# Performance work log

Measured on AMD Instinct MI355X. Metric: run time of the kernel, lower is better.

Reference implementation:

```python
import jax, jax.numpy as jnp
import numpy as np

B, C, H, W = 8, 256, 64, 64
CI = 128  # inter_channels
EPS = 1e-5

def conv1x1(x, w, b):
    # x:[B,C,H,W], w:[O,C], b:[O] -> [B,O,H,W]
    return jnp.einsum('bchw,oc->bohw', x, w) + b[None, :, None, None]

def maxpool2(t):
    b, c, h, w = t.shape
    return t.reshape(b, c, h // 2, 2, w // 2, 2).max(axis=(3, 5))

def setup_inputs() -> dict:
    key = jax.random.key(0)
    ks = jax.random.split(key, 11)
    s_in = 1.0 / np.sqrt(C)
    s_ci = 1.0 / np.sqrt(CI)
    return {
        'x':        jax.random.normal(ks[0], (B, C, H, W), jnp.float32),
        'g_w':      jax.random.normal(ks[1], (CI, C), jnp.float32) * s_in,
        'g_b':      jax.random.normal(ks[2], (CI,), jnp.float32) * s_in,
        'theta_w':  jax.random.normal(ks[3], (CI, C), jnp.float32) * s_in,
        'theta_b':  jax.random.normal(ks[4], (CI,), jnp.float32) * s_in,
        'phi_w':    jax.random.normal(ks[5], (CI, C), jnp.float32) * s_in,
        'phi_b':    jax.random.normal(ks[6], (CI,), jnp.float32) * s_in,
        'w_w':      jax.random.normal(ks[7], (C, CI), jnp.float32) * s_ci,
        'w_b':      jax.random.normal(ks[8], (C,), jnp.float32) * s_ci,
        'bn_gamma': jax.random.normal(ks[9], (C,), jnp.float32) * 0.1 + 1.0,
        'bn_beta':  jax.random.normal(ks[10], (C,), jnp.float32) * 0.1,
    }

def reference(x, g_w, g_b, theta_w, theta_b, phi_w, phi_b, w_w, w_b, bn_gamma, bn_beta):
    b, c, h, w = x.shape
    n = h * w
    # g and phi are sub-sampled with 2x2 max pool -> Ns = n // 4
    g_x = maxpool2(conv1x1(x, g_w, g_b)).reshape(b, CI, -1)      # [B,CI,Ns]
    g_x = g_x.transpose(0, 2, 1)                                  # [B,Ns,CI]
    theta_x = conv1x1(x, theta_w, theta_b).reshape(b, CI, n)
    theta_x = theta_x.transpose(0, 2, 1)                          # [B,N,CI]
    phi_x = maxpool2(conv1x1(x, phi_w, phi_b)).reshape(b, CI, -1)  # [B,CI,Ns]
    f = jnp.einsum('bnc,bcm->bnm', theta_x, phi_x)                # [B,N,Ns] (no 1/sqrt(d) scale, faithful)
    f_div_c = jax.nn.softmax(f, axis=-1)
    y = jnp.einsum('bnm,bmc->bnc', f_div_c, g_x)                  # [B,N,CI]
    y = y.transpose(0, 2, 1).reshape(b, CI, h, w)
    wy = conv1x1(y, w_w, w_b)                                     # [B,C,H,W]
    # BatchNorm2d in training mode: batch stats over (B,H,W)
    mean = wy.mean(axis=(0, 2, 3), keepdims=True)
    var = wy.var(axis=(0, 2, 3), keepdims=True)
    wy_bn = (wy - mean) * jax.lax.rsqrt(var + EPS)
    wy_bn = wy_bn * bn_gamma[None, :, None, None] + bn_beta[None, :, None, None]
    return wy_bn + x
```

## Files before the change

### kernel.cpp

```cpp
#include <hip/hip_runtime.h>
#include <hip/hip_bf16.h>
#include <hip/hip_fp16.h>
#include <math.h>

#define B 8
#define C 256
#define HH 64
#define WW 64
#define NN 4096
#define CI 128
#define NS 1024
#define EPS 1e-5f

typedef __attribute__((ext_vector_type(8))) _Float16 f16x8;
typedef __attribute__((ext_vector_type(4))) float f32x4;

static __device__ __forceinline__ unsigned short f2h_bits(float f) {
    return __half_as_ushort(__float2half(f));
}
static __device__ __forceinline__ float h2f(unsigned short u) {
    return __half2float(__ushort_as_half(u));
}

__global__ __launch_bounds__(256) void k_xt(const float* __restrict__ x,
        unsigned short* __restrict__ xh,
        const float* __restrict__ tw, const float* __restrict__ pw,
        const float* __restrict__ gw, const float* __restrict__ ww,
        unsigned short* __restrict__ wh) {
    int tid = threadIdx.x;
    if (blockIdx.x == 64) {
        int inst = blockIdx.y * B + blockIdx.z;
        int base = inst * 4096;
        #pragma unroll
        for (int k = 0; k < 16; ++k) {
            int idx = base + tid + k * 256;
            int sel = idx >> 15, off = idx & 32767;
            const float* src = (sel == 0) ? tw : (sel == 1) ? pw : (sel == 2) ? gw : ww;
            wh[idx] = f2h_bits(src[off]);
        }
        return;
    }
    __shared__ float s_t[64 * 65];
    int n0 = blockIdx.x * 64;
    int c0 = blockIdx.y * 64;
    int b  = blockIdx.z;
    #pragma unroll
    for (int k = 0; k < 16; ++k) {
        int idx = tid + k * 256;
        int cl = idx >> 6, nl = idx & 63;
        s_t[cl * 65 + nl] = x[((size_t)b * C + c0 + cl) * NN + n0 + nl];
    }
    __syncthreads();
    #pragma unroll
    for (int k = 0; k < 8; ++k) {
        int idx = tid + k * 256;
        int nl = idx >> 5, cp = (idx & 31) * 2;
        ushort2 o;
        o.x = f2h_bits(s_t[cp * 65 + nl]);
        o.y = f2h_bits(s_t[(cp + 1) * 65 + nl]);
        *(ushort2*)&xh[((size_t)b * NN + n0 + nl) * C + c0 + cp] = o;
    }
}

__global__ __launch_bounds__(512) void k_convs(const unsigned short* __restrict__ xh,
        const unsigned short* __restrict__ twh, const unsigned short* __restrict__ pwh,
        const unsigned short* __restrict__ gwh,
        const float* __restrict__ tb, const float* __restrict__ pb, const float* __restrict__ gb_,
        unsigned short* __restrict__ theta, unsigned short* __restrict__ phi,
        unsigned short* __restrict__ gout) {
    int blk = blockIdx.x;
    int b   = blk >> 5;
    int mh  = blk & 31;
    int tid = threadIdx.x;
    int lane = tid & 63, wv = tid >> 6;
    int lr = lane & 15, lh = lane >> 4;
    int wn = wv & 3, wc = wv >> 2;
    size_t row0 = (size_t)blk * 128;

    f32x4 accT[8];
    f32x4 aP0[4], aP1[4], aG0[4], aG1[4];
    #pragma unroll
    for (int i = 0; i < 8; ++i) accT[i] = (f32x4){0,0,0,0};
    #pragma unroll
    for (int i = 0; i < 4; ++i) {
        aP0[i] = (f32x4){0,0,0,0}; aP1[i] = (f32x4){0,0,0,0};
        aG0[i] = (f32x4){0,0,0,0}; aG1[i] = (f32x4){0,0,0,0};
    }

    const unsigned short* ap0 = xh + (row0 + wn * 16 + lr) * C + lh * 8;
    const unsigned short* ap1 = ap0 + (size_t)64 * C;
    #pragma unroll
    for (int kc = 0; kc < 8; ++kc) {
        f16x8 a0 = *(const f16x8*)(ap0 + kc * 32);
        f16x8 a1 = *(const f16x8*)(ap1 + kc * 32);
        f16x8 aT = (wv < 4) ? a0 : a1;
        #pragma unroll
        for (int ct = 0; ct < 8; ++ct) {
            f16x8 bt_ = *(const f16x8*)&twh[(ct * 16 + lr) * C + kc * 32 + lh * 8];
            accT[ct] = __builtin_amdgcn_mfma_f32_16x16x32_f16(aT, bt_, accT[ct], 0, 0, 0);
        }
        #pragma unroll
        for (int ct = 0; ct < 4; ++ct) {
            int wrow = (wc * 64 + ct * 16 + lr) * C + kc * 32 + lh * 8;
            f16x8 bp = *(const f16x8*)&pwh[wrow];
            f16x8 bg = *(const f16x8*)&gwh[wrow];
            aP0[ct] = __builtin_amdgcn_mfma_f32_16x16x32_f16(a0, bp, aP0[ct], 0, 0, 0);
            aP1[ct] = __builtin_amdgcn_mfma_f32_16x16x32_f16(a1, bp, aP1[ct], 0, 0, 0);
            aG0[ct] = __builtin_amdgcn_mfma_f32_16x16x32_f16(a0, bg, aG0[ct], 0, 0, 0);
            aG1[ct] = __builtin_amdgcn_mfma_f32_16x16x32_f16(a1, bg, aG1[ct], 0, 0, 0);
        }
    }
    #pragma unroll
    for (int ct = 0; ct < 8; ++ct) {
        int ci = ct * 16 + lr;
        float bias = tb[ci];
        #pragma unroll
        for (int r = 0; r < 4; ++r)
            theta[(row0 + wv * 16 + lh * 4 + r) * CI + ci] = f2h_bits(accT[ct][r] + bias);
    }
    #pragma unroll
    for (int ct = 0; ct < 4; ++ct) {
        int ci = wc * 64 + ct * 16 + lr;
        float biasP = pb[ci], biasG = gb_[ci];
        #pragma unroll
        for (int j = 0; j < 2; ++j) {
            int m = mh * 32 + wn * 8 + lh * 2 + j;
            float vP = fmaxf(fmaxf(aP0[ct][2*j], aP0[ct][2*j+1]),
                             fmaxf(aP1[ct][2*j], aP1[ct][2*j+1])) + biasP;
            float vG = fmaxf(fmaxf(aG0[ct][2*j], aG0[ct][2*j+1]),
                             fmaxf(aG1[ct][2*j], aG1[ct][2*j+1])) + biasG;
            phi[((size_t)b * NS + m) * CI + ci]  = f2h_bits(vP);
            gout[((size_t)b * CI + ci) * NS + m] = f2h_bits(vG);
        }
    }
}

#define SPH 136
#define SG  72
#define SP  72
__global__ __launch_bounds__(256, 3) void k_attn_mfma(const unsigned short* __restrict__ theta,
        const unsigned short* __restrict__ phi, const unsigned short* __restrict__ g,
        unsigned short* __restrict__ yp, float2* __restrict__ ml) {
    __shared__ unsigned short s_ph[64 * SPH];
    __shared__ unsigned short s_g[128 * SG];
    __shared__ unsigned short s_p[64 * SP];
    int rb = blockIdx.x;
    int b  = blockIdx.y;
    int sx = blockIdx.z;
    int tid = threadIdx.x;
    int lane = tid & 63, wv = tid >> 6;
    int lr = lane & 15, lh = lane >> 4;
    int row0 = rb * 64;
    int wrow = wv * 16;

    f16x8 a_th[4];
    {
        const unsigned short* tp = theta + ((size_t)b * NN + row0 + wrow + lr) * CI + lh * 8;
        #pragma unroll
        for (int kc = 0; kc < 4; ++kc) a_th[kc] = *(const f16x8*)(tp + kc * 32);
    }

    f32x4 yacc[8];
    #pragma unroll
    for (int i = 0; i < 8; ++i) yacc[i] = (f32x4){0.f, 0.f, 0.f, 0.f};
    float mrun[4] = {-1e30f, -1e30f, -1e30f, -1e30f};
    float lrun[4] = {0.f, 0.f, 0.f, 0.f};

    for (int t = 0; t < 8; ++t) {
        int mt = sx * 8 + t;
        __syncthreads();
        {
            const ushort4* src = (const ushort4*)(phi + ((size_t)b * NS + mt * 64) * CI);
            #pragma unroll
            for (int k = 0; k < 8; ++k) {
                int tt = tid + k * 256;
                int r = tt >> 5, cq = tt & 31;
                ushort4 vv = src[r * 32 + cq];
                *(ushort4*)&s_ph[r * SPH + cq * 4] = vv;
            }
            const ushort4* sg = (const ushort4*)(g + (size_t)b * CI * NS);
            #pragma unroll
            for (int k = 0; k < 8; ++k) {
                int tt = tid + k * 256;
                int ci = tt >> 4, cq = tt & 15;
                ushort4 vv = sg[ci * 256 + mt * 16 + cq];
                *(ushort4*)&s_g[ci * SG + cq * 4] = vv;
            }
        }
        __syncthreads();

        f32x4 S[4];
        #pragma unroll
        for (int nt = 0; nt < 4; ++nt) S[nt] = (f32x4){0.f, 0.f, 0.f, 0.f};
        #pragma unroll
        for (int nt = 0; nt < 4; ++nt) {
            #pragma unroll
            for (int kc = 0; kc < 4; ++kc) {
                f16x8 bf = *(const f16x8*)&s_ph[(nt * 16 + lr) * SPH + kc * 32 + lh * 8];
                S[nt] = __builtin_amdgcn_mfma_f32_16x16x32_f16(a_th[kc], bf, S[nt], 0, 0, 0);
            }
        }

        float rmax[4], rs[4], scale[4];
        #pragma unroll
        for (int r = 0; r < 4; ++r)
            rmax[r] = fmaxf(fmaxf(S[0][r], S[1][r]), fmaxf(S[2][r], S[3][r]));
        #pragma unroll
        for (int s = 1; s < 16; s <<= 1) {
            #pragma unroll
            for (int r = 0; r < 4; ++r) rmax[r] = fmaxf(rmax[r], __shfl_xor(rmax[r], s));
        }
        #pragma unroll
        for (int r = 0; r < 4; ++r) {
            float mnew = fmaxf(mrun[r], rmax[r]);
            scale[r] = __expf(mrun[r] - mnew);
            mrun[r] = mnew;
            rs[r] = 0.f;
        }
        #pragma unroll
        for (int nt = 0; nt < 4; ++nt) {
            #pragma unroll
            for (int r = 0; r < 4; ++r) {
                float e = __expf(S[nt][r] - mrun[r]);
                S[nt][r] = e;
                rs[r] += e;
            }
        }
        #pragma unroll
        for (int s = 1; s < 16; s <<= 1) {
            #pragma unroll
            for (int r = 0; r < 4; ++r) rs[r] += __shfl_xor(rs[r], s);
        }
        #pragma unroll
        for (int r = 0; r < 4; ++r) lrun[r] = lrun[r] * scale[r] + rs[r];
        #pragma unroll
        for (int i = 0; i < 8; ++i) {
            #pragma unroll
            for (int r = 0; r < 4; ++r) yacc[i][r] *= scale[r];
        }
        #pragma unroll
        for (int nt = 0; nt < 4; ++nt) {
            #pragma unroll
            for (int r = 0; r < 4; ++r)
                s_p[(wrow + lh * 4 + r) * SP + nt * 16 + lr] = f2h_bits(S[nt][r]);
        }

        f16x8 a_p[2];
        #pragma unroll
        for (int kc = 0; kc < 2; ++kc)
            a_p[kc] = *(const f16x8*)&s_p[(wrow + lr) * SP + kc * 32 + lh * 8];
        #pragma unroll
        for (int ct = 0; ct < 8; ++ct) {
            #pragma unroll
            for (int kc = 0; kc < 2; ++kc) {
                f16x8 bg = *(const f16x8*)&s_g[(ct * 16 + lr) * SG + kc * 32 + lh * 8];
                yacc[ct] = __builtin_amdgcn_mfma_f32_16x16x32_f16(a_p[kc], bg, yacc[ct], 0, 0, 0);
            }
        }
    }

    size_t pbase = ((size_t)(sx * B + b) * NN + row0 + wrow);
    #pragma unroll
    for (int ct = 0; ct < 8; ++ct) {
        #pragma unroll
        for (int r = 0; r < 4; ++r)
            yp[(pbase + lh * 4 + r) * CI + ct * 16 + lr] = f2h_bits(yacc[ct][r]);
    }
    if (lr == 0) {
        #pragma unroll
        for (int r = 0; r < 4; ++r) {
            float2 v; v.x = mrun[r]; v.y = lrun[r];
            ml[pbase + lh * 4 + r] = v;
        }
    }
}

__global__ __launch_bounds__(256) void k_wconv(const unsigned short* __restrict__ yp,
        const float2* __restrict__ ml, const unsigned short* __restrict__ wwh,
        const float* __restrict__ wb, unsigned short* __restrict__ wyh,
        float* __restrict__ psum, float* __restrict__ psq) {
    int blk = blockIdx.x;
    int b   = blk >> 6;
    int nloc = (blk & 63) * 64;
    int tid = threadIdx.x;
    int lane = tid & 63, wv = tid >> 6;
    int lr = lane & 15, lh = lane >> 4;

    f32x4 acc[4][4];
    #pragma unroll
    for (int i = 0; i < 4; ++i)
        #pragma unroll
        for (int j = 0; j < 4; ++j) acc[i][j] = (f32x4){0.f, 0.f, 0.f, 0.f};

    const unsigned short* y0b = yp + ((size_t)b * NN + nloc) * CI;
    const unsigned short* y1b = yp + ((size_t)(B + b) * NN + nloc) * CI;
    const float2* ml0 = ml + ((size_t)b * NN + nloc);
    const float2* ml1 = ml + ((size_t)(B + b) * NN + nloc);

    float a0v[4], a1v[4];
    #pragma unroll
    for (int bt = 0; bt < 4; ++bt) {
        int n = bt * 16 + lr;
        float2 p0 = ml0[n], p1 = ml1[n];
        float M = fmaxf(p0.x, p1.x);
        float e0 = __expf(p0.x - M), e1 = __expf(p1.x - M);
        float L = e0 * p0.y + e1 * p1.y;
        a0v[bt] = e0 / L;
        a1v[bt] = e1 / L;
    }

    #pragma unroll
    for (int kc = 0; kc < 4; ++kc) {
        f16x8 a[4], bf[4];
        #pragma unroll
        for (int at = 0; at < 4; ++at)
            a[at] = *(const f16x8*)&wwh[(wv * 64 + at * 16 + lr) * CI + kc * 32 + lh * 8];
        #pragma unroll
        for (int bt = 0; bt < 4; ++bt) {
            size_t off = (size_t)(bt * 16 + lr) * CI + kc * 32 + lh * 8;
            f16x8 u0 = *(const f16x8*)&y0b[off];
            f16x8 u1 = *(const f16x8*)&y1b[off];
            f16x8 v;
            #pragma unroll
            for (int i = 0; i < 8; ++i)
                v[i] = (_Float16)(a0v[bt] * (float)u0[i] + a1v[bt] * (float)u1[i]);
            bf[bt] = v;
        }
        #pragma unroll
        for (int at = 0; at < 4; ++at)
            #pragma unroll
            for (int bt = 0; bt < 4; ++bt)
                acc[at][bt] = __builtin_amdgcn_mfma_f32_16x16x32_f16(a[at], bf[bt], acc[at][bt], 0, 0, 0);
    }
    #pragma unroll
    for (int at = 0; at < 4; ++at) {
        #pragma unroll
        for (int r = 0; r < 4; ++r) {
            int co = wv * 64 + at * 16 + lh * 4 + r;
            float bias = wb[co];
            unsigned short* wp = wyh + ((size_t)b * C + co) * NN + nloc;
            float sv = 0.f, q = 0.f;
            #pragma unroll
            for (int bt = 0; bt < 4; ++bt) {
                float v = acc[at][bt][r] + bias;
                wp[bt * 16 + lr] = f2h_bits(v);
                sv += v;
                q = fmaf(v, v, q);
            }
            #pragma unroll
            for (int o = 1; o < 16; o <<= 1) {
                sv += __shfl_xor(sv, o);
                q  += __shfl_xor(q, o);
            }
            if (lr == 0) {
                psum[co * 512 + blk] = sv;
                psq[co * 512 + blk]  = q;
            }
        }
    }
}

__global__ __launch_bounds__(64) void k_stats_r(const float* __restrict__ psum,
        const float* __restrict__ psq, float* __restrict__ stats) {
    int c = blockIdx.x;
    int lane = threadIdx.x;
    float s = 0.f, q = 0.f;
    #pragma unroll
    for (int k = 0; k < 8; ++k) {
        s += psum[c * 512 + lane + k * 64];
        q += psq[c * 512 + lane + k * 64];
    }
    #pragma unroll
    for (int o = 32; o >= 1; o >>= 1) {
        s += __shfl_down(s, o);
        q += __shfl_down(q, o);
    }
    if (lane == 0) { stats[c] = s; stats[256 + c] = q; }
}

__global__ __launch_bounds__(256) void k_bn_out(const unsigned short* __restrict__ wyh,
        const float* __restrict__ x, const float* __restrict__ stats,
        const float* __restrict__ gamma, const float* __restrict__ beta,
        float* __restrict__ out) {
    size_t t = (size_t)blockIdx.x * 256 + threadIdx.x;
    size_t base = t * 8;
    int c = (int)((base >> 12) & 255);
    float mean = stats[c] * (1.f / 32768.f);
    float var  = stats[256 + c] * (1.f / 32768.f) - mean * mean;
    float sc = gamma[c] * rsqrtf(var + EPS);
    float sh = beta[c] - mean * sc;
    ushort4 w0 = *(const ushort4*)&wyh[base];
    ushort4 w1 = *(const ushort4*)&wyh[base + 4];
    float4 x0 = *(const float4*)&x[base];
    float4 x1 = *(const float4*)&x[base + 4];
    float4 o0, o1;
    o0.x = fmaf(h2f(w0.x), sc, sh) + x0.x;
    o0.y = fmaf(h2f(w0.y), sc, sh) + x0.y;
    o0.z = fmaf(h2f(w0.z), sc, sh) + x0.z;
    o0.w = fmaf(h2f(w0.w), sc, sh) + x0.w;
    o1.x = fmaf(h2f(w1.x), sc, sh) + x1.x;
    o1.y = fmaf(h2f(w1.y), sc, sh) + x1.y;
    o1.z = fmaf(h2f(w1.z), sc, sh) + x1.z;
    o1.w = fmaf(h2f(w1.w), sc, sh) + x1.w;
    *(float4*)&out[base]     = o0;
    *(float4*)&out[base + 4] = o1;
}

extern "C" void kernel_launch(void* const* d_in, const int* in_sizes, int n_in,
                              void* d_out, int out_size, void* d_ws, size_t ws_size,
                              hipStream_t stream) {
    const float* x    = (const float*)d_in[0];
    const float* g_w  = (const float*)d_in[1];
    const float* g_b  = (const float*)d_in[2];
    const float* th_w = (const float*)d_in[3];
    const float* th_b = (const float*)d_in[4];
    const float* ph_w = (const float*)d_in[5];
    const float* ph_b = (const float*)d_in[6];
    const float* w_w  = (const float*)d_in[7];
    const float* w_b  = (const float*)d_in[8];
    const float* bn_g = (const float*)d_in[9];
    const float* bn_b = (const float*)d_in[10];
    float* out = (float*)d_out;

    char* w0 = (char*)d_ws;
    unsigned short* xh    = (unsigned short*)w0;
    unsigned short* yp    = (unsigned short*)w0;
    unsigned short* theta = (unsigned short*)(w0 + 16777216);
    unsigned short* wh    = (unsigned short*)(w0 + 25165824);
    unsigned short* twh   = wh;
    unsigned short* pwh   = wh + 32768;
    unsigned short* gwh   = wh + 65536;
    unsigned short* wwh   = wh + 98304;
    unsigned short* phi   = (unsigned short*)(w0 + 25427968);
    unsigned short* gx    = (unsigned short*)(w0 + 27525120);
    unsigned short* wyh   = (unsigned short*)(w0 + 38010880);
    float*          psum  = (float*)(w0 + 54788096);
    float*          psq   = (float*)(w0 + 55312384);
    float*          stats = (float*)(w0 + 55836672);
    float2*         ml    = (float2*)(w0 + 55840768);

    k_xt<<<dim3(65, 4, B), 256, 0, stream>>>(x, xh, th_w, ph_w, g_w, w_w, wh);
    k_convs<<<256, 512, 0, stream>>>(xh, twh, pwh, gwh, th_b, ph_b, g_b, theta, phi, gx);
    k_attn_mfma<<<dim3(64, B, 2), 256, 0, stream>>>(theta, phi, gx, yp, ml);
    k_wconv<<<512, 256, 0, stream>>>(yp, ml, wwh, w_b, wyh, psum, psq);
    k_stats_r<<<256, 64, 0, stream>>>(psum, psq, stats);
    k_bn_out<<<4096, 256, 0, stream>>>(wyh, x, stats, bn_g, bn_b, out);
}
```

Measured before the change: 135.6 us.

## Prefetch next phi/g tile into registers during MFMA compute in attention kernel

Global loads of the phi and g tiles for the next iteration now go into registers before the current tile's MFMA work, and are written to shared memory after it. The goal is to hide global-memory latency behind compute instead of stalling at the top of each iteration. s_setprio also raises wave priority around the MFMA blocks. This costs 16 extra ushort4 registers per thread, which may lower occupancy.

```diff
diff --git a/kernel.cpp b/kernel.cpp
--- a/kernel.cpp
+++ b/kernel.cpp
@@ -160,38 +160,44 @@
         for (int kc = 0; kc < 4; ++kc) a_th[kc] = *(const f16x8*)(tp + kc * 32);
     }
 
+    const ushort4* phsrc = (const ushort4*)(phi + (size_t)b * NS * CI);
+    const ushort4* gsrc  = (const ushort4*)(g + (size_t)b * CI * NS);
+
+    ushort4 rph[8], rg[8];
+    auto issue = [&](int mt) {
+        #pragma unroll
+        for (int k = 0; k < 8; ++k) {
+            int tt = tid + k * 256;
+            rph[k] = phsrc[(mt * 64 + (tt >> 5)) * 32 + (tt & 31)];
+            rg[k]  = gsrc[(tt >> 4) * 256 + mt * 16 + (tt & 15)];
+        }
+    };
+    auto commit = [&]() {
+        #pragma unroll
+        for (int k = 0; k < 8; ++k) {
+            int tt = tid + k * 256;
+            *(ushort4*)&s_ph[(tt >> 5) * SPH + (tt & 31) * 4] = rph[k];
+            *(ushort4*)&s_g[(tt >> 4) * SG + (tt & 15) * 4]   = rg[k];
+        }
+    };
+
     f32x4 yacc[8];
     #pragma unroll
     for (int i = 0; i < 8; ++i) yacc[i] = (f32x4){0.f, 0.f, 0.f, 0.f};
     float mrun[4] = {-1e30f, -1e30f, -1e30f, -1e30f};
     float lrun[4] = {0.f, 0.f, 0.f, 0.f};
 
+    issue(sx * 8);
+    commit();
+    __syncthreads();
+
     for (int t = 0; t < 8; ++t) {
-        int mt = sx * 8 + t;
-        __syncthreads();
-        {
-            const ushort4* src = (const ushort4*)(phi + ((size_t)b * NS + mt * 64) * CI);
-            #pragma unroll
-            for (int k = 0; k < 8; ++k) {
-                int tt = tid + k * 256;
-                int r = tt >> 5, cq = tt & 31;
-                ushort4 vv = src[r * 32 + cq];
-                *(ushort4*)&s_ph[r * SPH + cq * 4] = vv;
-            }
-            const ushort4* sg = (const ushort4*)(g + (size_t)b * CI * NS);
-            #pragma unroll
-            for (int k = 0; k < 8; ++k) {
-                int tt = tid + k * 256;
-                int ci = tt >> 4, cq = tt & 15;
-                ushort4 vv = sg[ci * 256 + mt * 16 + cq];
-                *(ushort4*)&s_g[ci * SG + cq * 4] = vv;
-            }
-        }
-        __syncthreads();
+        if (t < 7) issue(sx * 8 + t + 1);
 
         f32x4 S[4];
         #pragma unroll
         for (int nt = 0; nt < 4; ++nt) S[nt] = (f32x4){0.f, 0.f, 0.f, 0.f};
+        __builtin_amdgcn_s_setprio(1);
         #pragma unroll
         for (int nt = 0; nt < 4; ++nt) {
             #pragma unroll
@@ -200,6 +206,7 @@
                 S[nt] = __builtin_amdgcn_mfma_f32_16x16x32_f16(a_th[kc], bf, S[nt], 0, 0, 0);
             }
         }
+        __builtin_amdgcn_s_setprio(0);
 
         float rmax[4], rs[4], scale[4];
         #pragma unroll
@@ -249,6 +256,7 @@
         #pragma unroll
         for (int kc = 0; kc < 2; ++kc)
             a_p[kc] = *(const f16x8*)&s_p[(wrow + lr) * SP + kc * 32 + lh * 8];
+        __builtin_amdgcn_s_setprio(1);
         #pragma unroll
         for (int ct = 0; ct < 8; ++ct) {
             #pragma unroll
@@ -256,6 +264,13 @@
                 f16x8 bg = *(const f16x8*)&s_g[(ct * 16 + lr) * SG + kc * 32 + lh * 8];
                 yacc[ct] = __builtin_amdgcn_mfma_f32_16x16x32_f16(a_p[kc], bg, yacc[ct], 0, 0, 0);
             }
+        }
+        __builtin_amdgcn_s_setprio(0);
+
+        __syncthreads();
+        if (t < 7) {
+            commit();
+            __syncthreads();
         }
     }
 
```

Measured after the change: 136.5 us. No clear change (+0.6%).

## Split attention key dimension four ways and merge partials in output conv

Applied to the files above, without the earlier changes.

The flash-attention kernel now splits the key/value dimension into four chunks instead of two, doubling the grid to 2048 blocks with half as many tiles per block. The output 1x1 conv kernel merges four partial results using the stored max and sum values. The workspace layout is reshuffled so the larger partial-output buffer fits. The intent is more parallelism and occupancy in attention. The cost is twice the partial-output write and read traffic and more merge work in the conv kernel.

```diff
diff --git a/kernel.cpp b/kernel.cpp
--- a/kernel.cpp
+++ b/kernel.cpp
@@ -11,6 +11,7 @@
 #define CI 128
 #define NS 1024
 #define EPS 1e-5f
+#define MSPLIT 4
 
 typedef __attribute__((ext_vector_type(8))) _Float16 f16x8;
 typedef __attribute__((ext_vector_type(4))) float f32x4;
@@ -166,8 +167,8 @@
     float mrun[4] = {-1e30f, -1e30f, -1e30f, -1e30f};
     float lrun[4] = {0.f, 0.f, 0.f, 0.f};
 
-    for (int t = 0; t < 8; ++t) {
-        int mt = sx * 8 + t;
+    for (int t = 0; t < 4; ++t) {
+        int mt = sx * 4 + t;
         __syncthreads();
         {
             const ushort4* src = (const ushort4*)(phi + ((size_t)b * NS + mt * 64) * CI);
@@ -292,21 +293,35 @@
         #pragma unroll
         for (int j = 0; j < 4; ++j) acc[i][j] = (f32x4){0.f, 0.f, 0.f, 0.f};
 
-    const unsigned short* y0b = yp + ((size_t)b * NN + nloc) * CI;
-    const unsigned short* y1b = yp + ((size_t)(B + b) * NN + nloc) * CI;
-    const float2* ml0 = ml + ((size_t)b * NN + nloc);
-    const float2* ml1 = ml + ((size_t)(B + b) * NN + nloc);
-
-    float a0v[4], a1v[4];
+    const unsigned short* ybs[MSPLIT];
+    const float2* mls[MSPLIT];
+    #pragma unroll
+    for (int s = 0; s < MSPLIT; ++s) {
+        ybs[s] = yp + ((size_t)(s * B + b) * NN + nloc) * CI;
+        mls[s] = ml + ((size_t)(s * B + b) * NN + nloc);
+    }
+
+    float av[MSPLIT][4];
     #pragma unroll
     for (int bt = 0; bt < 4; ++bt) {
         int n = bt * 16 + lr;
-        float2 p0 = ml0[n], p1 = ml1[n];
-        float M = fmaxf(p0.x, p1.x);
-        float e0 = __expf(p0.x - M), e1 = __expf(p1.x - M);
-        float L = e0 * p0.y + e1 * p1.y;
-        a0v[bt] = e0 / L;
-        a1v[bt] = e1 / L;
+        float mx[MSPLIT], lv[MSPLIT];
+        float M = -1e30f;
+        #pragma unroll
+        for (int s = 0; s < MSPLIT; ++s) {
+            float2 p = mls[s][n];
+            mx[s] = p.x; lv[s] = p.y;
+            M = fmaxf(M, p.x);
+        }
+        float L = 0.f, ev[MSPLIT];
+        #pragma unroll
+        for (int s = 0; s < MSPLIT; ++s) {
+            ev[s] = __expf(mx[s] - M);
+            L = fmaf(ev[s], lv[s], L);
+        }
+        float invL = 1.f / L;
+        #pragma unroll
+        for (int s = 0; s < MSPLIT; ++s) av[s][bt] = ev[s] * invL;
     }
 
     #pragma unroll
@@ -318,12 +333,18 @@
         #pragma unroll
         for (int bt = 0; bt < 4; ++bt) {
             size_t off = (size_t)(bt * 16 + lr) * CI + kc * 32 + lh * 8;
-            f16x8 u0 = *(const f16x8*)&y0b[off];
-            f16x8 u1 = *(const f16x8*)&y1b[off];
+            float vf[8];
+            #pragma unroll
+            for (int i = 0; i < 8; ++i) vf[i] = 0.f;
+            #pragma unroll
+            for (int s = 0; s < MSPLIT; ++s) {
+                f16x8 u = *(const f16x8*)&ybs[s][off];
+                #pragma unroll
+                for (int i = 0; i < 8; ++i) vf[i] = fmaf(av[s][bt], (float)u[i], vf[i]);
+            }
             f16x8 v;
             #pragma unroll
-            for (int i = 0; i < 8; ++i)
-                v[i] = (_Float16)(a0v[bt] * (float)u0[i] + a1v[bt] * (float)u1[i]);
+            for (int i = 0; i < 8; ++i) v[i] = (_Float16)vf[i];
             bf[bt] = v;
         }
         #pragma unroll
@@ -424,7 +445,7 @@
 
     char* w0 = (char*)d_ws;
     unsigned short* xh    = (unsigned short*)w0;
-    unsigned short* yp    = (unsigned short*)w0;
+    unsigned short* wyh   = (unsigned short*)w0;
     unsigned short* theta = (unsigned short*)(w0 + 16777216);
     unsigned short* wh    = (unsigned short*)(w0 + 25165824);
     unsigned short* twh   = wh;
@@ -433,15 +454,15 @@
     unsigned short* wwh   = wh + 98304;
     unsigned short* phi   = (unsigned short*)(w0 + 25427968);
     unsigned short* gx    = (unsigned short*)(w0 + 27525120);
-    unsigned short* wyh   = (unsigned short*)(w0 + 38010880);
-    float*          psum  = (float*)(w0 + 54788096);
-    float*          psq   = (float*)(w0 + 55312384);
-    float*          stats = (float*)(w0 + 55836672);
-    float2*         ml    = (float2*)(w0 + 55840768);
+    unsigned short* yp    = (unsigned short*)(w0 + 29622272);
+    float*          psum  = (float*)(w0 + 63176704);
+    float*          psq   = (float*)(w0 + 63700992);
+    float*          stats = (float*)(w0 + 64225280);
+    float2*         ml    = (float2*)(w0 + 64227328);
 
     k_xt<<<dim3(65, 4, B), 256, 0, stream>>>(x, xh, th_w, ph_w, g_w, w_w, wh);
     k_convs<<<256, 512, 0, stream>>>(xh, twh, pwh, gwh, th_b, ph_b, g_b, theta, phi, gx);
-    k_attn_mfma<<<dim3(64, B, 2), 256, 0, stream>>>(theta, phi, gx, yp, ml);
+    k_attn_mfma<<<dim3(64, B, MSPLIT), 256, 0, stream>>>(theta, phi, gx, yp, ml);
     k_wconv<<<512, 256, 0, stream>>>(yp, ml, wwh, w_b, wyh, psum, psq);
     k_stats_r<<<256, 64, 0, stream>>>(psum, psq, stats);
     k_bn_out<<<4096, 256, 0, stream>>>(wyh, x, stats, bn_g, bn_b, out);
```

Result: slower. 141.0 us (+4.0%).
